# Optimization experiments

Hardware: AMD Instinct MI355X
Metric: run time of the kernel (lower is better)

Reference implementation:

```python
import jax, jax.numpy as jnp
import numpy as np

B, S, D_IN, D_OUT, H = 2, 2048, 1024, 1024, 16
HD = D_OUT // H  # 64


def setup_inputs() -> dict:
    key = jax.random.key(0)
    k1, k2, k3, k4 = jax.random.split(key, 4)
    x = jax.random.normal(k1, (B, S, D_IN), dtype=jnp.float32)
    # Linear weights stored pre-transposed as [d_in, d_out] so y = x @ W
    sc = 1.0 / np.sqrt(D_IN)
    Wq = jax.random.normal(k2, (D_IN, D_OUT), dtype=jnp.float32) * sc
    Wk = jax.random.normal(k3, (D_IN, D_OUT), dtype=jnp.float32) * sc
    Wv = jax.random.normal(k4, (D_IN, D_OUT), dtype=jnp.float32) * sc
    return {"x": x, "Wq": Wq, "Wk": Wk, "Wv": Wv}


def reference(x, Wq, Wk, Wv):
    b, s, _ = x.shape
    # project and split heads: [B, S, H, HD]
    q = (x @ Wq).reshape(b, s, H, HD)
    k = (x @ Wk).reshape(b, s, H, HD)
    v = (x @ Wv).reshape(b, s, H, HD)
    # scores: [B, H, Sq, Sk]
    scores = jnp.einsum("bqhd,bkhd->bhqk", q, k)
    # causal mask: triu(ones, diagonal=1) -> mask positions where k > q
    causal = jnp.triu(jnp.ones((s, s), dtype=bool), k=1)
    scores = jnp.where(causal, -jnp.inf, scores)
    # FAITHFUL quirks: scale by sqrt(d_out) (full model dim) and
    # softmax over dim=2 = the QUERY axis of [B, H, Sq, Sk]
    scale = jnp.float32(D_OUT) ** 0.5
    weights = jax.nn.softmax(scores / scale, axis=2)
    # context: [B, H, Sq, HD] -> [B, Sq, H*HD]
    ctx = jnp.einsum("bhqk,bhkd->bhqd", weights, v.transpose(0, 2, 1, 3))
    return ctx.transpose(0, 2, 1, 3).reshape(b, s, H * HD)
```

## Files before the change

kernel.cpp:

```cpp
#include <hip/hip_runtime.h>
#include <hip/hip_bf16.h>


typedef __attribute__((ext_vector_type(8))) short short8;
typedef __attribute__((ext_vector_type(4))) float floatx4;

#define SS 2048
#define DIN 1024
#define DOUT 1024
#define NH 16
#define HD 64
#define QSCALE 0.04508422002778011f

#define MFMA16(a,b,c) __builtin_amdgcn_mfma_f32_16x16x32_bf16((a),(b),(c),0,0,0)
#define EXP2F(x) __builtin_amdgcn_exp2f(x)

__device__ __forceinline__ void gl_lds16(const void* g, void* l) {
  __builtin_amdgcn_global_load_lds((const __attribute__((address_space(1))) void*)g,
                                   (__attribute__((address_space(3))) void*)l, 16, 0, 0);
}

__device__ __forceinline__ void stage64(const __hip_bfloat16* __restrict__ src, int stride,
                                        __hip_bfloat16* lds, int c, int l) {
  int r = c * 8 + (l >> 3);
  int cc = ((l & 7) ^ ((l >> 3) & 7)) * 8;
  gl_lds16(src + (size_t)r * stride + cc, lds + c * 512);
}

__device__ __forceinline__ short8 frag64(const __hip_bfloat16* lds, int row, int ks, int l) {
  return *(const short8*)&lds[row * 64 + (((ks * 4 + (l >> 4)) ^ (row & 7)) * 8)];
}

__global__ __launch_bounds__(256) void k_cvt_x(const float* __restrict__ x,
                                               __hip_bfloat16* __restrict__ xb) {
  size_t i = ((size_t)blockIdx.x * 256 + threadIdx.x) * 4;
  float4 v = *(const float4*)(x + i);
  union { __hip_bfloat16 h[4]; short4 s; } u;
  u.h[0] = __float2bfloat16(v.x); u.h[1] = __float2bfloat16(v.y);
  u.h[2] = __float2bfloat16(v.z); u.h[3] = __float2bfloat16(v.w);
  *(short4*)(xb + i) = u.s;
}

__global__ void k_twb(const float* __restrict__ W, __hip_bfloat16* __restrict__ Wt) {
  __shared__ float t[32][33];
  int tx = threadIdx.x, ty = threadIdx.y;
  int k0 = blockIdx.y * 32, c0 = blockIdx.x * 32;
#pragma unroll
  for (int i = 0; i < 4; ++i)
    t[ty + 8*i][tx] = W[(size_t)(k0 + ty + 8*i) * DOUT + c0 + tx];
  __syncthreads();
#pragma unroll
  for (int i = 0; i < 4; ++i)
    Wt[(size_t)(c0 + ty + 8*i) * DIN + k0 + tx] = __float2bfloat16(t[tx][ty + 8*i]);
}

__global__ __launch_bounds__(256) void k_qkv(
    const __hip_bfloat16* __restrict__ xb,
    const __hip_bfloat16* __restrict__ wq, const __hip_bfloat16* __restrict__ wk,
    const __hip_bfloat16* __restrict__ wv,
    __hip_bfloat16* __restrict__ qb, __hip_bfloat16* __restrict__ kb,
    __hip_bfloat16* __restrict__ vb) {
  __shared__ __hip_bfloat16 smem[32768];

  const __hip_bfloat16* wt; __hip_bfloat16* outp;
  if (blockIdx.z == 0)      { wt = wq; outp = qb; }
  else if (blockIdx.z == 1) { wt = wk; outp = kb; }
  else                      { wt = wv; outp = vb; }

  const int tid = threadIdx.x, w = tid >> 6, l = tid & 63;
  const int row0 = blockIdx.y * 128, col0 = blockIdx.x * 128;
  const int mw = (w >> 1) * 64, nw = (w & 1) * 64;

  const floatx4 fz = {0.f, 0.f, 0.f, 0.f};
  floatx4 acc[4][4];
#pragma unroll
  for (int m = 0; m < 4; ++m)
#pragma unroll
    for (int n = 0; n < 4; ++n) acc[m][n] = fz;

#pragma unroll
  for (int i = 0; i < 4; ++i) {
    stage64(xb + (size_t)row0 * DIN, DIN, smem, w*4+i, l);
    stage64(wt + (size_t)col0 * DIN, DIN, smem + 16384, w*4+i, l);
  }
  __syncthreads();

  for (int kt = 0; kt < 16; ++kt) {
    int cur = kt & 1;
    __hip_bfloat16* Ac = smem + cur * 8192;
    __hip_bfloat16* Bc = smem + 16384 + cur * 8192;
    if (kt < 15) {
      int kk = (kt + 1) * 64;
      __hip_bfloat16* An = smem + (cur ^ 1) * 8192;
      __hip_bfloat16* Bn = smem + 16384 + (cur ^ 1) * 8192;
#pragma unroll
      for (int i = 0; i < 4; ++i) {
        stage64(xb + (size_t)row0 * DIN + kk, DIN, An, w*4+i, l);
        stage64(wt + (size_t)col0 * DIN + kk, DIN, Bn, w*4+i, l);
      }
    }
    short8 a[4][2], b[4][2];
#pragma unroll
    for (int m = 0; m < 4; ++m)
#pragma unroll
      for (int ks = 0; ks < 2; ++ks)
        a[m][ks] = frag64(Ac, mw + m*16 + (l & 15), ks, l);
#pragma unroll
    for (int n = 0; n < 4; ++n)
#pragma unroll
      for (int ks = 0; ks < 2; ++ks)
        b[n][ks] = frag64(Bc, nw + n*16 + (l & 15), ks, l);
#pragma unroll
    for (int ks = 0; ks < 2; ++ks)
#pragma unroll
      for (int m = 0; m < 4; ++m)
#pragma unroll
        for (int n = 0; n < 4; ++n)
          acc[m][n] = MFMA16(a[m][ks], b[n][ks], acc[m][n]);
    __syncthreads();
  }

  if (blockIdx.z == 2) {
    __hip_bfloat16* Vt2 = smem;
#pragma unroll
    for (int m = 0; m < 4; ++m)
#pragma unroll
      for (int n = 0; n < 4; ++n)
#pragma unroll
        for (int r4 = 0; r4 < 4; ++r4) {
          int r = mw + m*16 + ((l >> 4) << 2) + r4;
          int c = nw + n*16 + (l & 15);
          Vt2[c * 136 + r] = __float2bfloat16(acc[m][n][r4]);
        }
    __syncthreads();
    int bb2 = row0 >> 11, sbase = row0 & (SS - 1);
#pragma unroll
    for (int i = 0; i < 8; ++i) {
      int drow = (tid >> 4) + i * 16;
      int scol = (tid & 15) * 8;
      int colg = col0 + drow, hh = colg >> 6, d = colg & 63;
      *(short8*)(outp + (((size_t)bb2 * NH + hh) * HD + d) * SS + sbase + scol) =
          *(const short8*)&Vt2[drow * 136 + scol];
    }
  } else {
    float sc = (blockIdx.z == 0) ? QSCALE : 1.0f;
#pragma unroll
    for (int m = 0; m < 4; ++m)
#pragma unroll
      for (int n = 0; n < 4; ++n)
#pragma unroll
        for (int r4 = 0; r4 < 4; ++r4) {
          int row = row0 + mw + m*16 + ((l >> 4) << 2) + r4;
          int col = col0 + nw + n*16 + (l & 15);
          int bb2 = row >> 11, s = row & (SS - 1), hh = col >> 6, d = col & 63;
          outp[(((size_t)bb2 * NH + hh) * SS + s) * HD + d] =
              __float2bfloat16(acc[m][n][r4] * sc);
        }
  }
}

__global__ __launch_bounds__(256) void k_cstat(const __hip_bfloat16* __restrict__ qb,
                                               const __hip_bfloat16* __restrict__ kb,
                                               __hip_bfloat16* __restrict__ vtb) {
  __shared__ __hip_bfloat16 smem[20480];
  __shared__ float red[4][64];
  __shared__ float zl[64];
  __hip_bfloat16* Kt = smem;
  const int bh = blockIdx.x;
  const int tid = threadIdx.x, w = tid >> 6, l = tid & 63;

  for (int jj = 0; jj < 2; ++jj) {
    int j = jj ? (31 - (int)blockIdx.y) : (int)blockIdx.y;
    int k0 = j * 64;
    int t0 = k0 >> 7, niter = 16 - t0;

#pragma unroll
    for (int i = 0; i < 2; ++i)
      stage64(kb + ((size_t)bh * SS + k0) * HD, HD, Kt, w*2+i, l);
#pragma unroll
    for (int i = 0; i < 4; ++i)
      stage64(qb + ((size_t)bh * SS + (t0 << 7)) * HD, HD, smem + 4096, w*4+i, l);
    __syncthreads();

    short8 kf[4][2];
#pragma unroll
    for (int n = 0; n < 4; ++n)
#pragma unroll
      for (int ks = 0; ks < 2; ++ks)
        kf[n][ks] = frag64(Kt, n*16 + (l & 15), ks, l);

    float csum[4] = {0.f, 0.f, 0.f, 0.f};
    for (int it = 0; it < niter; ++it) {
      int cur = it & 1;
      __hip_bfloat16* Qc = smem + 4096 + cur * 8192;
      int q0 = (t0 + it) << 7;
      if (it + 1 < niter) {
        __hip_bfloat16* Qn = smem + 4096 + (cur ^ 1) * 8192;
#pragma unroll
        for (int i = 0; i < 4; ++i)
          stage64(qb + ((size_t)bh * SS + q0 + 128) * HD, HD, Qn, w*4+i, l);
      }
      int qw = q0 + w * 32;
      if (qw + 31 >= k0) {
        short8 qa[2][2];
#pragma unroll
        for (int mm = 0; mm < 2; ++mm)
#pragma unroll
          for (int ks = 0; ks < 2; ++ks)
            qa[mm][ks] = frag64(Qc, w*32 + mm*16 + (l & 15), ks, l);
        floatx4 s[2][4];
#pragma unroll
        for (int mm = 0; mm < 2; ++mm)
#pragma unroll
          for (int n = 0; n < 4; ++n) {
            floatx4 t = {0.f, 0.f, 0.f, 0.f};
#pragma unroll
            for (int ks = 0; ks < 2; ++ks) t = MFMA16(qa[mm][ks], kf[n][ks], t);
            s[mm][n] = t;
          }
        bool dia = (k0 + 63 > qw);
#pragma unroll
        for (int mm = 0; mm < 2; ++mm)
#pragma unroll
          for (int n = 0; n < 4; ++n)
#pragma unroll
            for (int r4 = 0; r4 < 4; ++r4) {
              float e = EXP2F(s[mm][n][r4]);
              if (dia) {
                int q = qw + mm*16 + ((l >> 4) << 2) + r4;
                int k = k0 + n*16 + (l & 15);
                if (k > q) e = 0.f;
              }
              csum[n] += e;
            }
      }
      __syncthreads();
    }

#pragma unroll
    for (int n = 0; n < 4; ++n) {
      csum[n] += __shfl_xor(csum[n], 16);
      csum[n] += __shfl_xor(csum[n], 32);
      if (l < 16) red[w][n*16 + l] = csum[n];
    }
    __syncthreads();
    if (tid < 64)
      zl[tid] = 1.0f / (red[0][tid] + red[1][tid] + red[2][tid] + red[3][tid]);
    __syncthreads();
#pragma unroll
    for (int i = 0; i < 4; ++i) {
      int d = (tid >> 4) + i * 16;
      int c = (tid & 15) * 4;
      size_t base = ((size_t)bh * HD + d) * SS + k0 + c;
      short4 v = *(const short4*)(vtb + base);
      __hip_bfloat16* hp = (__hip_bfloat16*)&v;
#pragma unroll
      for (int jv = 0; jv < 4; ++jv)
        hp[jv] = __float2bfloat16(__bfloat162float(hp[jv]) * zl[c + jv]);
      *(short4*)(vtb + base) = v;
    }
    __syncthreads();
  }
}

__global__ __launch_bounds__(512) void k_ctx(const __hip_bfloat16* __restrict__ qb,
                                             const __hip_bfloat16* __restrict__ kb,
                                             const __hip_bfloat16* __restrict__ vtb,
                                             float* __restrict__ outp) {
  __shared__ __hip_bfloat16 smem[32768];
  const int bh = blockIdx.x, bb = bh >> 4, h = bh & 15;
  const int by = blockIdx.y;
  const int tid = threadIdx.x, w = tid >> 6, l = tid & 63;
  const int Tbig = 15 - by, Tsml = by;
  const int myT = (w < 4) ? Tbig : Tsml;
  const int q0 = myT * 128;
  const int qw = q0 + (w & 3) * 32;
  const int nkt = Tbig * 2 + 2;

#pragma unroll
  for (int i = 0; i < 2; ++i) {
    stage64(qb + ((size_t)bh * SS + Tbig * 128) * HD, HD, smem,        w*2+i, l);
    stage64(qb + ((size_t)bh * SS + Tsml * 128) * HD, HD, smem + 8192, w*2+i, l);
  }
  stage64(kb + (size_t)bh * SS * HD, HD, smem + 16384, w, l);
  stage64(vtb + (size_t)bh * HD * SS, SS, smem + 24576, w, l);
  __syncthreads();

  short8 qa[2][2];
  {
    const __hip_bfloat16* Qt = smem + ((w < 4) ? 0 : 8192);
#pragma unroll
    for (int mm = 0; mm < 2; ++mm)
#pragma unroll
      for (int ks = 0; ks < 2; ++ks)
        qa[mm][ks] = frag64(Qt, (w & 3)*32 + mm*16 + (l & 15), ks, l);
  }
  __syncthreads();
  __hip_bfloat16* Pt = smem + w * 2048;

  const floatx4 fz = {0.f, 0.f, 0.f, 0.f};
  floatx4 acc[2][4];
#pragma unroll
  for (int mm = 0; mm < 2; ++mm)
#pragma unroll
    for (int dn = 0; dn < 4; ++dn) acc[mm][dn] = fz;

  for (int kt = 0; kt < nkt; ++kt) {
    int cur = kt & 1;
    __hip_bfloat16* Kc = smem + 16384 + cur * 4096;
    __hip_bfloat16* Vc = smem + 24576 + cur * 4096;
    int k0 = kt << 6;
    if (kt + 1 < nkt) {
      int kn = k0 + 64;
      stage64(kb + ((size_t)bh * SS + kn) * HD, HD, smem + 16384 + (cur^1) * 4096, w, l);
      stage64(vtb + (size_t)bh * HD * SS + kn, SS, smem + 24576 + (cur^1) * 4096, w, l);
    }
    if (k0 < qw + 32) {
      floatx4 s[2][4];
#pragma unroll
      for (int mm = 0; mm < 2; ++mm)
#pragma unroll
        for (int n = 0; n < 4; ++n) {
          floatx4 t = {0.f, 0.f, 0.f, 0.f};
#pragma unroll
          for (int ks = 0; ks < 2; ++ks)
            t = MFMA16(qa[mm][ks], frag64(Kc, n*16 + (l & 15), ks, l), t);
          s[mm][n] = t;
        }
      bool dia = (k0 + 63 > qw);
#pragma unroll
      for (int mm = 0; mm < 2; ++mm)
#pragma unroll
        for (int n = 0; n < 4; ++n)
#pragma unroll
          for (int r4 = 0; r4 < 4; ++r4) {
            float p = EXP2F(s[mm][n][r4]);
            if (dia) {
              int q = qw + mm*16 + ((l >> 4) << 2) + r4;
              int k = k0 + n*16 + (l & 15);
              if (k > q) p = 0.f;
            }
            int rl = mm*16 + ((l >> 4) << 2) + r4;
            Pt[rl * 64 + ((n*16 + (l & 15)) ^ ((rl & 7) << 3))] = __float2bfloat16(p);
          }
#pragma unroll
      for (int mm = 0; mm < 2; ++mm)
#pragma unroll
        for (int ks = 0; ks < 2; ++ks) {
          short8 pa = frag64(Pt, mm*16 + (l & 15), ks, l);
#pragma unroll
          for (int dn = 0; dn < 4; ++dn)
            acc[mm][dn] = MFMA16(pa, frag64(Vc, dn*16 + (l & 15), ks, l), acc[mm][dn]);
        }
    }
    __syncthreads();
  }

#pragma unroll
  for (int mm = 0; mm < 2; ++mm)
#pragma unroll
    for (int dn = 0; dn < 4; ++dn)
#pragma unroll
      for (int r4 = 0; r4 < 4; ++r4) {
        int q = qw + mm*16 + ((l >> 4) << 2) + r4;
        outp[((size_t)bb * SS + q) * DOUT + h * HD + dn*16 + (l & 15)] = acc[mm][dn][r4];
      }
}

extern "C" void kernel_launch(void* const* d_in, const int* in_sizes, int n_in,
                              void* d_out, int out_size, void* d_ws, size_t ws_size,
                              hipStream_t stream) {
  const float* x  = (const float*)d_in[0];
  const float* Wq = (const float*)d_in[1];
  const float* Wk = (const float*)d_in[2];
  const float* Wv = (const float*)d_in[3];
  float* out = (float*)d_out;
  char* ws = (char*)d_ws;

  __hip_bfloat16* xb  = (__hip_bfloat16*)(ws);
  __hip_bfloat16* wtq = (__hip_bfloat16*)(ws + (8ull  << 20));
  __hip_bfloat16* wtk = (__hip_bfloat16*)(ws + (10ull << 20));
  __hip_bfloat16* wtv = (__hip_bfloat16*)(ws + (12ull << 20));
  __hip_bfloat16* qb  = (__hip_bfloat16*)(ws + (14ull << 20));
  __hip_bfloat16* kb  = (__hip_bfloat16*)(ws + (22ull << 20));
  __hip_bfloat16* vtb = (__hip_bfloat16*)(ws + (30ull << 20));

  k_cvt_x<<<4096, 256, 0, stream>>>(x, xb);
  dim3 tb(32, 8);
  k_twb<<<dim3(32, 32), tb, 0, stream>>>(Wq, wtq);
  k_twb<<<dim3(32, 32), tb, 0, stream>>>(Wk, wtk);
  k_twb<<<dim3(32, 32), tb, 0, stream>>>(Wv, wtv);
  k_qkv<<<dim3(8, 32, 3), 256, 0, stream>>>(xb, wtq, wtk, wtv, qb, kb, vtb);
  k_cstat<<<dim3(32, 16), 256, 0, stream>>>(qb, kb, vtb);
  k_ctx<<<dim3(32, 8), 512, 0, stream>>>(qb, kb, vtb, out);
}
```

Baseline: 119.0 us.

## Use 32x32 MFMA with transposed scores and register-resident P in ctx kernel

```diff
diff --git a/kernel.cpp b/kernel.cpp
--- a/kernel.cpp
+++ b/kernel.cpp
@@ -4,6 +4,7 @@
 
 typedef __attribute__((ext_vector_type(8))) short short8;
 typedef __attribute__((ext_vector_type(4))) float floatx4;
+typedef __attribute__((ext_vector_type(16))) float floatx16;
 
 #define SS 2048
 #define DIN 1024
@@ -13,6 +14,7 @@
 #define QSCALE 0.04508422002778011f
 
 #define MFMA16(a,b,c) __builtin_amdgcn_mfma_f32_16x16x32_bf16((a),(b),(c),0,0,0)
+#define MFMA32(a,b,c) __builtin_amdgcn_mfma_f32_32x32x16_bf16((a),(b),(c),0,0,0)
 #define EXP2F(x) __builtin_amdgcn_exp2f(x)
 
 __device__ __forceinline__ void gl_lds16(const void* g, void* l) {
@@ -29,6 +31,10 @@
 
 __device__ __forceinline__ short8 frag64(const __hip_bfloat16* lds, int row, int ks, int l) {
   return *(const short8*)&lds[row * 64 + (((ks * 4 + (l >> 4)) ^ (row & 7)) * 8)];
+}
+
+__device__ __forceinline__ short8 frag32(const __hip_bfloat16* lds, int row, int subk, int l) {
+  return *(const short8*)&lds[row * 64 + (((subk * 2 + (l >> 5)) ^ (row & 7)) * 8)];
 }
 
 __global__ __launch_bounds__(256) void k_cvt_x(const float* __restrict__ x,
@@ -267,104 +273,100 @@
                                              const __hip_bfloat16* __restrict__ kb,
                                              const __hip_bfloat16* __restrict__ vtb,
                                              float* __restrict__ outp) {
-  __shared__ __hip_bfloat16 smem[32768];
+  __shared__ __hip_bfloat16 smem[16384];
   const int bh = blockIdx.x, bb = bh >> 4, h = bh & 15;
   const int by = blockIdx.y;
   const int tid = threadIdx.x, w = tid >> 6, l = tid & 63;
+  const int hi = l >> 5;
   const int Tbig = 15 - by, Tsml = by;
   const int myT = (w < 4) ? Tbig : Tsml;
-  const int q0 = myT * 128;
-  const int qw = q0 + (w & 3) * 32;
+  const int q0w = myT * 128 + (w & 3) * 32;
   const int nkt = Tbig * 2 + 2;
 
-#pragma unroll
-  for (int i = 0; i < 2; ++i) {
-    stage64(qb + ((size_t)bh * SS + Tbig * 128) * HD, HD, smem,        w*2+i, l);
-    stage64(qb + ((size_t)bh * SS + Tsml * 128) * HD, HD, smem + 8192, w*2+i, l);
-  }
-  stage64(kb + (size_t)bh * SS * HD, HD, smem + 16384, w, l);
-  stage64(vtb + (size_t)bh * HD * SS, SS, smem + 24576, w, l);
+  short8 qf[4];
+  {
+    const __hip_bfloat16* qrow = qb + ((size_t)bh * SS + q0w + (l & 31)) * HD + hi * 8;
+#pragma unroll
+    for (int hc = 0; hc < 4; ++hc)
+      qf[hc] = *(const short8*)(qrow + hc * 16);
+  }
+
+  stage64(kb + (size_t)bh * SS * HD, HD, smem, w, l);
+  stage64(vtb + (size_t)bh * HD * SS, SS, smem + 8192, w, l);
   __syncthreads();
 
-  short8 qa[2][2];
-  {
-    const __hip_bfloat16* Qt = smem + ((w < 4) ? 0 : 8192);
-#pragma unroll
-    for (int mm = 0; mm < 2; ++mm)
-#pragma unroll
-      for (int ks = 0; ks < 2; ++ks)
-        qa[mm][ks] = frag64(Qt, (w & 3)*32 + mm*16 + (l & 15), ks, l);
-  }
-  __syncthreads();
-  __hip_bfloat16* Pt = smem + w * 2048;
-
-  const floatx4 fz = {0.f, 0.f, 0.f, 0.f};
-  floatx4 acc[2][4];
-#pragma unroll
-  for (int mm = 0; mm < 2; ++mm)
-#pragma unroll
-    for (int dn = 0; dn < 4; ++dn) acc[mm][dn] = fz;
+  const floatx16 fz16 = {0,0,0,0,0,0,0,0,0,0,0,0,0,0,0,0};
+  floatx16 acc[2];
+  acc[0] = fz16; acc[1] = fz16;
 
   for (int kt = 0; kt < nkt; ++kt) {
     int cur = kt & 1;
-    __hip_bfloat16* Kc = smem + 16384 + cur * 4096;
-    __hip_bfloat16* Vc = smem + 24576 + cur * 4096;
+    __hip_bfloat16* Kc = smem + cur * 4096;
+    __hip_bfloat16* Vc = smem + 8192 + cur * 4096;
     int k0 = kt << 6;
     if (kt + 1 < nkt) {
       int kn = k0 + 64;
-      stage64(kb + ((size_t)bh * SS + kn) * HD, HD, smem + 16384 + (cur^1) * 4096, w, l);
-      stage64(vtb + (size_t)bh * HD * SS + kn, SS, smem + 24576 + (cur^1) * 4096, w, l);
-    }
-    if (k0 < qw + 32) {
-      floatx4 s[2][4];
-#pragma unroll
-      for (int mm = 0; mm < 2; ++mm)
-#pragma unroll
-        for (int n = 0; n < 4; ++n) {
-          floatx4 t = {0.f, 0.f, 0.f, 0.f};
-#pragma unroll
-          for (int ks = 0; ks < 2; ++ks)
-            t = MFMA16(qa[mm][ks], frag64(Kc, n*16 + (l & 15), ks, l), t);
-          s[mm][n] = t;
-        }
-      bool dia = (k0 + 63 > qw);
-#pragma unroll
-      for (int mm = 0; mm < 2; ++mm)
-#pragma unroll
-        for (int n = 0; n < 4; ++n)
-#pragma unroll
-          for (int r4 = 0; r4 < 4; ++r4) {
-            float p = EXP2F(s[mm][n][r4]);
+      stage64(kb + ((size_t)bh * SS + kn) * HD, HD, smem + (cur^1) * 4096, w, l);
+      stage64(vtb + (size_t)bh * HD * SS + kn, SS, smem + 8192 + (cur^1) * 4096, w, l);
+    }
+    if (k0 < q0w + 32) {
+      floatx16 st[2];
+#pragma unroll
+      for (int H = 0; H < 2; ++H) {
+        floatx16 t = fz16;
+#pragma unroll
+        for (int hc = 0; hc < 4; ++hc)
+          t = MFMA32(frag32(Kc, H*32 + (l & 31), hc, l), qf[hc], t);
+        st[H] = t;
+      }
+      const bool dia = (k0 + 63 > q0w);
+      const int qg = q0w + (l & 31);
+      unsigned pk[2][4][2];
+#pragma unroll
+      for (int H = 0; H < 2; ++H)
+#pragma unroll
+        for (int m = 0; m < 4; ++m)
+#pragma unroll
+          for (int pr = 0; pr < 2; ++pr) {
+            float e0 = EXP2F(st[H][m*4 + pr*2]);
+            float e1 = EXP2F(st[H][m*4 + pr*2 + 1]);
             if (dia) {
-              int q = qw + mm*16 + ((l >> 4) << 2) + r4;
-              int k = k0 + n*16 + (l & 15);
-              if (k > q) p = 0.f;
+              int kb0 = k0 + H*32 + m*8 + hi*4 + pr*2;
+              if (kb0 > qg)     e0 = 0.f;
+              if (kb0 + 1 > qg) e1 = 0.f;
             }
-            int rl = mm*16 + ((l >> 4) << 2) + r4;
-            Pt[rl * 64 + ((n*16 + (l & 15)) ^ ((rl & 7) << 3))] = __float2bfloat16(p);
+            pk[H][m][pr] = (unsigned)__bfloat16_as_ushort(__float2bfloat16(e0)) |
+                           ((unsigned)__bfloat16_as_ushort(__float2bfloat16(e1)) << 16);
           }
 #pragma unroll
-      for (int mm = 0; mm < 2; ++mm)
-#pragma unroll
-        for (int ks = 0; ks < 2; ++ks) {
-          short8 pa = frag64(Pt, mm*16 + (l & 15), ks, l);
-#pragma unroll
-          for (int dn = 0; dn < 4; ++dn)
-            acc[mm][dn] = MFMA16(pa, frag64(Vc, dn*16 + (l & 15), ks, l), acc[mm][dn]);
-        }
-    }
-    __syncthreads();
-  }
-
-#pragma unroll
-  for (int mm = 0; mm < 2; ++mm)
-#pragma unroll
-    for (int dn = 0; dn < 4; ++dn)
-#pragma unroll
-      for (int r4 = 0; r4 < 4; ++r4) {
-        int q = qw + mm*16 + ((l >> 4) << 2) + r4;
-        outp[((size_t)bb * SS + q) * DOUT + h * HD + dn*16 + (l & 15)] = acc[mm][dn][r4];
-      }
+      for (int ks = 0; ks < 4; ++ks) {
+        const int H = ks >> 1, mb = (ks & 1) * 2;
+        unsigned keep0 = hi ? pk[H][mb+1][0] : pk[H][mb][0];
+        unsigned keep1 = hi ? pk[H][mb+1][1] : pk[H][mb][1];
+        unsigned send0 = hi ? pk[H][mb][0]   : pk[H][mb+1][0];
+        unsigned send1 = hi ? pk[H][mb][1]   : pk[H][mb+1][1];
+        unsigned recv0 = (unsigned)__shfl_xor((int)send0, 32);
+        unsigned recv1 = (unsigned)__shfl_xor((int)send1, 32);
+        union { unsigned u[4]; short8 s; } pa;
+        pa.u[0] = hi ? recv0 : keep0;
+        pa.u[1] = hi ? recv1 : keep1;
+        pa.u[2] = hi ? keep0 : recv0;
+        pa.u[3] = hi ? keep1 : recv1;
+#pragma unroll
+        for (int dn = 0; dn < 2; ++dn)
+          acc[dn] = MFMA32(pa.s, frag32(Vc, dn*32 + (l & 31), ks, l), acc[dn]);
+      }
+    }
+    __syncthreads();
+  }
+
+#pragma unroll
+  for (int dn = 0; dn < 2; ++dn)
+#pragma unroll
+    for (int r = 0; r < 16; ++r) {
+      int q = q0w + (r & 3) + 8*(r >> 2) + 4*hi;
+      outp[((size_t)bb * SS + q) * DOUT + h * HD + dn*32 + (l & 31)] = acc[dn][r];
+    }
 }
 
 extern "C" void kernel_launch(void* const* d_in, const int* in_sizes, int n_in,
```

Result: slower. 122.4 us (+2.9%).
